# Kernel optimization log

Hardware: AMD Instinct MI355X
Metric: run time of the kernel (lower is better)

Reference implementation:

```python
import jax, jax.numpy as jnp
import numpy as np

D_MODEL = 256; D_INNER = 512; D_STATE = 32; D_CONV = 4
NHEADS = 8; HEADDIM = 64; NLAYERS = 2
CONV_DIM = D_INNER + 2 * D_STATE          # 576
ZX = 2 * D_INNER + 2 * D_STATE + NHEADS   # 1096
BSZ = 4; SEQ = 2048
EPS = 1e-5


def _causal_conv(x, w, b):
    # depthwise causal conv: x (b,l,c), w (c,k), b (c,)
    k = w.shape[1]
    L = x.shape[1]
    xp = jnp.pad(x, ((0, 0), (k - 1, 0), (0, 0)))
    out = jnp.zeros_like(x)
    for i in range(k):
        out = out + xp[:, i:i + L, :] * w[:, i]
    return out + b


def _mamba2(u, in_w, conv_w, conv_b, dt_bias, A_log, Dvec, gnorm_w, out_w):
    bsz, l, _ = u.shape
    zxbcdt = jnp.einsum('bld,ed->ble', u, in_w)  # (b,l,ZX)
    z = zxbcdt[..., :D_INNER]
    xBC = zxbcdt[..., D_INNER:D_INNER + CONV_DIM]
    dt = jax.nn.softplus(zxbcdt[..., D_INNER + CONV_DIM:] + dt_bias)  # (b,l,h)
    xBC = jax.nn.silu(_causal_conv(xBC, conv_w, conv_b))
    xs = xBC[..., :D_INNER].reshape(bsz, l, NHEADS, HEADDIM)
    Bm = xBC[..., D_INNER:D_INNER + D_STATE]   # (b,l,n)
    Cm = xBC[..., D_INNER + D_STATE:]          # (b,l,n)
    A = -jnp.exp(A_log)                         # (h,)
    dA = jnp.exp(dt * A)                        # (b,l,h)
    dtx = dt[..., None] * xs                    # (b,l,h,p)

    def step(h, inp):
        dA_t, dtx_t, B_t, C_t = inp
        h = h * dA_t[:, :, None, None] + dtx_t[..., None] * B_t[:, None, None, :]
        y_t = jnp.einsum('bhpn,bn->bhp', h, C_t)
        return h, y_t

    h0 = jnp.zeros((bsz, NHEADS, HEADDIM, D_STATE), u.dtype)
    _, ys = jax.lax.scan(step, h0, (dA.swapaxes(0, 1), dtx.swapaxes(0, 1),
                                    Bm.swapaxes(0, 1), Cm.swapaxes(0, 1)))
    y = ys.swapaxes(0, 1) + Dvec[None, None, :, None] * xs
    y = y.reshape(bsz, l, D_INNER)
    y = y * jax.nn.silu(z)                       # gated RMSNorm (Mamba2 default)
    y = y * jax.lax.rsqrt(jnp.mean(y * y, axis=-1, keepdims=True) + EPS) * gnorm_w
    return jnp.einsum('ble,de->bld', y, out_w)


def _encoder(x, padding_mask, in_w, conv_w, conv_b, dt_bias, A_log, Dvec,
             gnorm_w, out_w, ln_w, ln_b):
    mask = padding_mask[..., None]

    def ln(h):
        mu = jnp.mean(h, -1, keepdims=True)
        var = jnp.mean((h - mu) ** 2, -1, keepdims=True)
        return (h - mu) * jax.lax.rsqrt(var + EPS) * ln_w + ln_b

    for i in range(NLAYERS):
        h = ln(x)
        of = _mamba2(h, in_w[i, 0], conv_w[i, 0], conv_b[i, 0], dt_bias[i, 0],
                     A_log[i, 0], Dvec[i, 0], gnorm_w[i, 0], out_w[i, 0])
        ob = jnp.flip(_mamba2(jnp.flip(h, 1), in_w[i, 1], conv_w[i, 1],
                              conv_b[i, 1], dt_bias[i, 1], A_log[i, 1],
                              Dvec[i, 1], gnorm_w[i, 1], out_w[i, 1]), 1)
        x = x + jnp.where(mask, 0.0, of + ob)
    return jnp.where(mask, 0.0, ln(x))


def setup_inputs() -> dict:
    key = jax.random.key(0)
    ks = jax.random.split(key, 8)
    s = 0.02
    x = jax.random.normal(ks[0], (BSZ, SEQ, D_MODEL), jnp.float32)
    padding_mask = jax.random.randint(ks[1], (BSZ, SEQ), 0, 2) > 0
    in_w = jax.random.normal(ks[2], (NLAYERS, 2, ZX, D_MODEL), jnp.float32) * s
    conv_w = jax.random.normal(ks[3], (NLAYERS, 2, CONV_DIM, D_CONV), jnp.float32) * s
    conv_b = jnp.zeros((NLAYERS, 2, CONV_DIM), jnp.float32)
    dt_bias = jax.random.normal(ks[4], (NLAYERS, 2, NHEADS), jnp.float32) * 0.1
    A_log = jnp.log(jax.random.uniform(ks[5], (NLAYERS, 2, NHEADS), jnp.float32, 1.0, 16.0))
    Dvec = jnp.ones((NLAYERS, 2, NHEADS), jnp.float32)
    gnorm_w = jnp.ones((NLAYERS, 2, D_INNER), jnp.float32)
    out_w = jax.random.normal(ks[6], (NLAYERS, 2, D_MODEL, D_INNER), jnp.float32) * s
    ln_w = jnp.ones((D_MODEL,), jnp.float32)
    ln_b = jnp.zeros((D_MODEL,), jnp.float32)
    return {"x": x, "padding_mask": padding_mask, "in_w": in_w, "conv_w": conv_w,
            "conv_b": conv_b, "dt_bias": dt_bias, "A_log": A_log, "Dvec": Dvec,
            "gnorm_w": gnorm_w, "out_w": out_w, "ln_w": ln_w, "ln_b": ln_b}


def reference(x, padding_mask, in_w, conv_w, conv_b, dt_bias, A_log, Dvec,
              gnorm_w, out_w, ln_w, ln_b):
    return _encoder(x, padding_mask, in_w, conv_w, conv_b, dt_bias, A_log,
                    Dvec, gnorm_w, out_w, ln_w, ln_b)
```

## Files before the change

kernel.cpp:

```cpp
#include <hip/hip_runtime.h>
#include <hip/hip_bf16.h>
#include <math.h>

#define SEQL 2048
#define NB 4
#define DMm 256
#define DIi 512
#define DSs 32
#define NHH 8
#define HDD 64
#define CDD 576
#define ZXD 1096
#define ZXT 2192
#define NPAD 2304
#define NLAY 2
#define QC 64
#define NCH 32
#define RT 8192
#define EPSV 1e-5f

typedef __hip_bfloat16 bf16_t;
using short8 = __attribute__((ext_vector_type(8))) short;
using f32x4  = __attribute__((ext_vector_type(4))) float;

__device__ __forceinline__ float bf16bits2f(short u) {
  union { unsigned int i; float f; } v;
  v.i = ((unsigned int)(unsigned short)u) << 16;
  return v.f;
}

__device__ __forceinline__ int torig(int d, int c, int s) {
  int v = c * QC + s;
  return d ? (SEQL - 1 - v) : v;
}

__device__ __forceinline__ int is_masked(const void* mask, const int* mflag, int r) {
  return (*mflag) ? (int)(((const unsigned char*)mask)[r] != 0)
                  : (int)(((const int*)mask)[r] != 0);
}

__global__ void detect_mask(const unsigned char* __restrict__ m, int* __restrict__ flag) {
  __shared__ int any;
  if (threadIdx.x == 0) any = 0;
  __syncthreads();
  int a = 0;
  for (int i = threadIdx.x; i < RT; i += blockDim.x)
    if ((i & 3) && m[i]) a = 1;
  if (a) atomicOr(&any, 1);
  __syncthreads();
  if (threadIdx.x == 0) *flag = any;
}

__global__ void cvt_weights(const float* __restrict__ in_w, const float* __restrict__ out_w,
                            bf16_t* __restrict__ inw_bf, bf16_t* __restrict__ wcat_bf) {
  const int n1 = NLAY * NPAD * DMm;
  const int n2 = NLAY * DMm * 1024;
  for (int idx = blockIdx.x * blockDim.x + threadIdx.x; idx < n1 + n2; idx += gridDim.x * blockDim.x) {
    if (idx < n1) {
      int l = idx / (NPAD * DMm);
      int rem = idx % (NPAD * DMm);
      int r = rem / DMm, k = rem % DMm;
      inw_bf[idx] = __float2bfloat16(r < ZXT ? in_w[((size_t)l * ZXT + r) * DMm + k] : 0.f);
    } else {
      int j = idx - n1;
      int l = j / (DMm * 1024);
      int rem = j % (DMm * 1024);
      int dd = rem >> 10, k = rem & 1023;
      int dir = k >> 9, e = k & 511;
      wcat_bf[j] = __float2bfloat16(out_w[((size_t)((l * 2 + dir) * DMm) + dd) * DIi + e]);
    }
  }
}

__global__ void ln_kernel(const float* __restrict__ x, bf16_t* __restrict__ h,
                          const float* __restrict__ lnw, const float* __restrict__ lnb) {
  int r = blockIdx.x, lane = threadIdx.x;
  float4 v = ((const float4*)(x + (size_t)r * DMm))[lane];
  float s = v.x + v.y + v.z + v.w;
  #pragma unroll
  for (int o = 32; o; o >>= 1) s += __shfl_xor(s, o);
  float mu = s * (1.f / DMm);
  float d0 = v.x - mu, d1 = v.y - mu, d2 = v.z - mu, d3 = v.w - mu;
  float q = d0*d0 + d1*d1 + d2*d2 + d3*d3;
  #pragma unroll
  for (int o = 32; o; o >>= 1) q += __shfl_xor(q, o);
  float rstd = rsqrtf(q * (1.f / DMm) + EPSV);
  float4 w  = ((const float4*)lnw)[lane];
  float4 bb = ((const float4*)lnb)[lane];
  union { bf16_t o4[4]; uint2 u; } out;
  out.o4[0] = __float2bfloat16(d0 * rstd * w.x + bb.x);
  out.o4[1] = __float2bfloat16(d1 * rstd * w.y + bb.y);
  out.o4[2] = __float2bfloat16(d2 * rstd * w.z + bb.z);
  out.o4[3] = __float2bfloat16(d3 * rstd * w.w + bb.w);
  ((uint2*)(h + (size_t)r * DMm))[lane] = out.u;
}

__global__ void final_ln(const float* __restrict__ x, const void* __restrict__ mask,
                         const int* __restrict__ mflag,
                         const float* __restrict__ lnw, const float* __restrict__ lnb,
                         float* __restrict__ out) {
  int r = blockIdx.x, lane = threadIdx.x;
  float4 v = ((const float4*)(x + (size_t)r * DMm))[lane];
  float s = v.x + v.y + v.z + v.w;
  #pragma unroll
  for (int o = 32; o; o >>= 1) s += __shfl_xor(s, o);
  float mu = s * (1.f / DMm);
  float d0 = v.x - mu, d1 = v.y - mu, d2 = v.z - mu, d3 = v.w - mu;
  float q = d0*d0 + d1*d1 + d2*d2 + d3*d3;
  #pragma unroll
  for (int o = 32; o; o >>= 1) q += __shfl_xor(q, o);
  float rstd = rsqrtf(q * (1.f / DMm) + EPSV);
  float4 w  = ((const float4*)lnw)[lane];
  float4 bb = ((const float4*)lnb)[lane];
  float4 o4;
  if (is_masked(mask, mflag, r)) { o4.x = o4.y = o4.z = o4.w = 0.f; }
  else {
    o4.x = d0 * rstd * w.x + bb.x; o4.y = d1 * rstd * w.y + bb.y;
    o4.z = d2 * rstd * w.z + bb.z; o4.w = d3 * rstd * w.w + bb.w;
  }
  ((float4*)(out + (size_t)r * DMm))[lane] = o4;
}

__global__ __launch_bounds__(256) void gemm_in(const bf16_t* __restrict__ A,
    const bf16_t* __restrict__ Bw, bf16_t* __restrict__ zx, float* __restrict__ dtf) {
  __shared__ __align__(16) bf16_t As[128][72];
  __shared__ __align__(16) bf16_t Bs[128][72];
  int L = blockIdx.y * 18 + blockIdx.x;
  int qx = L & 7, jx = L >> 3;
  int Lp = qx * 144 + jx;
  int n0 = (Lp % 18) * 128, m0 = (Lp / 18) * 128;
  int tid = threadIdx.x, lane = tid & 63, wid = tid >> 6;
  int wm = wid >> 1, wn = wid & 1;
  f32x4 acc[4][4] = {};
  int sr = tid >> 1, sh = (tid & 1) * 32;
  for (int k0 = 0; k0 < DMm; k0 += 64) {
    #pragma unroll
    for (int i = 0; i < 4; i++) {
      *(short8*)&As[sr][sh + i * 8] = *(const short8*)(A + (size_t)(m0 + sr) * DMm + k0 + sh + i * 8);
      *(short8*)&Bs[sr][sh + i * 8] = *(const short8*)(Bw + (size_t)(n0 + sr) * DMm + k0 + sh + i * 8);
    }
    __syncthreads();
    #pragma unroll
    for (int kk = 0; kk < 2; kk++) {
      short8 af[4], bf[4];
      #pragma unroll
      for (int mi = 0; mi < 4; mi++)
        af[mi] = *(const short8*)&As[wm * 64 + mi * 16 + (lane & 15)][kk * 32 + (lane >> 4) * 8];
      #pragma unroll
      for (int ni = 0; ni < 4; ni++)
        bf[ni] = *(const short8*)&Bs[wn * 64 + ni * 16 + (lane & 15)][kk * 32 + (lane >> 4) * 8];
      #pragma unroll
      for (int mi = 0; mi < 4; mi++)
        #pragma unroll
        for (int ni = 0; ni < 4; ni++)
          acc[mi][ni] = __builtin_amdgcn_mfma_f32_16x16x32_bf16(af[mi], bf[ni], acc[mi][ni], 0, 0, 0);
    }
    __syncthreads();
  }
  #pragma unroll
  for (int mi = 0; mi < 4; mi++) {
    #pragma unroll
    for (int ni = 0; ni < 4; ni++) {
      int col = n0 + wn * 64 + ni * 16 + (lane & 15);
      if (col < ZXT) {
        #pragma unroll
        for (int j = 0; j < 4; j++) {
          int row = m0 + wm * 64 + mi * 16 + (lane >> 4) * 4 + j;
          float v = acc[mi][ni][j];
          zx[(size_t)row * ZXT + col] = __float2bfloat16(v);
          if (col >= 1088 && col < 1096)
            dtf[(size_t)row * NHH + (col - 1088)] = v;
          else if (col >= 2184)
            dtf[((size_t)RT + row) * NHH + (col - 2184)] = v;
        }
      }
    }
  }
}

__global__ __launch_bounds__(256) void gemm_out(const bf16_t* __restrict__ A, const bf16_t* __restrict__ Bw,
    float* __restrict__ C, int M, int N, int K, int ldc,
    const void* __restrict__ mask, const int* __restrict__ mflag) {
  __shared__ bf16_t As[64][40];
  __shared__ bf16_t Bs[64][40];
  int n0 = blockIdx.x * 64, m0 = blockIdx.y * 64;
  int tid = threadIdx.x, lane = tid & 63, wid = tid >> 6;
  f32x4 acc[4] = {};
  int sr = tid >> 2, sk = (tid & 3) * 8;
  for (int k0 = 0; k0 < K; k0 += 32) {
    short8 av = *(const short8*)(A + (size_t)(m0 + sr) * K + k0 + sk);
    *(short8*)&As[sr][sk] = av;
    short8 bv = *(const short8*)(Bw + (size_t)(n0 + sr) * K + k0 + sk);
    *(short8*)&Bs[sr][sk] = bv;
    __syncthreads();
    short8 af = *(const short8*)&As[wid * 16 + (lane & 15)][(lane >> 4) * 8];
    #pragma unroll
    for (int nt = 0; nt < 4; nt++) {
      short8 bf = *(const short8*)&Bs[nt * 16 + (lane & 15)][(lane >> 4) * 8];
      acc[nt] = __builtin_amdgcn_mfma_f32_16x16x32_bf16(af, bf, acc[nt], 0, 0, 0);
    }
    __syncthreads();
  }
  #pragma unroll
  for (int nt = 0; nt < 4; nt++) {
    int col = n0 + nt * 16 + (lane & 15);
    #pragma unroll
    for (int j = 0; j < 4; j++) {
      int row = m0 + wid * 16 + (lane >> 4) * 4 + j;
      if (!is_masked(mask, mflag, row)) C[(size_t)row * ldc + col] += acc[nt][j];
    }
  }
}

__global__ __launch_bounds__(256) void chunk_p1(const bf16_t* __restrict__ zx,
    const float* __restrict__ conv_w, const float* __restrict__ conv_b,
    const float* __restrict__ dtf, const float* __restrict__ dt_bias,
    const float* __restrict__ A_log, const float* __restrict__ Dvec,
    bf16_t* __restrict__ ybuf, bf16_t* __restrict__ Sbuf, float* __restrict__ lgbuf,
    float* __restrict__ Pbuf, bf16_t* __restrict__ cbuf, int layer) {
  int c = blockIdx.x, hd = blockIdx.y, b = blockIdx.z;
  int h = hd >> 1, d = hd & 1;
  int tid = threadIdx.x, lane = tid & 63, wid = tid >> 6;
  int rb = b * SEQL;
  __shared__ __align__(16) bf16_t Bs[QC][40];
  __shared__ __align__(16) bf16_t Cs[QC][40];
  __shared__ __align__(16) bf16_t Xt[QC][72];
  __shared__ __align__(16) char shraw[19968];
  bf16_t (*rawX)[64]  = (bf16_t(*)[64])shraw;
  bf16_t (*rawBC)[64] = (bf16_t(*)[64])(shraw + 8576);
  float (*cw4)[4]     = (float(*)[4])(shraw + 17152);
  float *cbv          = (float*)(shraw + 19200);
  bf16_t (*Ms)[72]    = (bf16_t(*)[72])shraw;
  bf16_t (*Btw)[72]   = (bf16_t(*)[72])(shraw + 9216);
  __shared__ float lam[QC], dts[QC], wss[QC];

  for (int i = tid; i < 67 * 8; i += 256) {
    int s = i >> 3, p0 = (i & 7) * 8;
    int v = c * QC + s - 3;
    short8 xv = {0,0,0,0,0,0,0,0}, bcv = {0,0,0,0,0,0,0,0};
    if (v >= 0) {
      int t = d ? (SEQL - 1 - v) : v;
      const bf16_t* rowp = zx + (size_t)(rb + t) * ZXT + d * ZXD + DIi;
      xv  = *(const short8*)(rowp + h * HDD + p0);
      bcv = *(const short8*)(rowp + 512 + p0);
    }
    *(short8*)&rawX[s][p0]  = xv;
    *(short8*)&rawBC[s][p0] = bcv;
  }
  if (tid < 128) {
    int cch = (tid < 64) ? (h * HDD + tid) : (512 + (tid - 64));
    const float* wp = conv_w + ((size_t)((layer * 2 + d) * CDD) + cch) * 4;
    *(float4*)cw4[tid] = *(const float4*)wp;
    cbv[tid] = conv_b[(layer * 2 + d) * CDD + cch];
  }
  if (tid < QC) {
    int ro = rb + torig(d, c, tid);
    size_t rr = (size_t)d * RT + ro;
    float xv = dtf[rr * NHH + h] + dt_bias[(layer * 2 + d) * NHH + h];
    float dtv = (xv > 20.f) ? xv : log1pf(expf(xv));
    float Ah = -expf(A_log[(layer * 2 + d) * NHH + h]);
    float la = dtv * Ah;
    dts[tid] = dtv;
    #pragma unroll
    for (int o = 1; o < 64; o <<= 1) { float vv = __shfl_up(la, o); if (tid >= o) la += vv; }
    lam[tid] = la;
    Pbuf[rr * NHH + h] = expf(la);
    float lq = __shfl(la, 63);
    wss[tid] = expf(lq - la) * dtv;
    if (tid == 63) lgbuf[((b * NHH + h) * 2 + d) * NCH + c] = la;
  }
  __syncthreads();

  for (int i = tid; i < QC * HDD; i += 256) {
    int s = i >> 6, p = i & 63;
    float a = cbv[p];
    #pragma unroll
    for (int ii = 0; ii < 4; ii++)
      a += __bfloat162float(rawX[s + ii][p]) * cw4[p][ii];
    a = a / (1.f + expf(-a));
    Xt[p][s] = __float2bfloat16(a);
  }
  for (int i = tid; i < QC * HDD; i += 256) {
    int s = i >> 6, q = i & 63;
    float a = cbv[64 + q];
    #pragma unroll
    for (int ii = 0; ii < 4; ii++)
      a += __bfloat162float(rawBC[s + ii][q]) * cw4[64 + q][ii];
    a = a / (1.f + expf(-a));
    bf16_t av = __float2bfloat16(a);
    if (q < DSs) Bs[s][q] = av; else Cs[s][q - DSs] = av;
  }
  __syncthreads();

  {
    short8 cf = *(const short8*)&Cs[wid * 16 + (lane & 15)][(lane >> 4) * 8];
    int sbase = lane & 15;
    #pragma unroll
    for (int sc = 0; sc < 4; sc++) {
      int s = sc * 16 + sbase;
      if (sc <= wid) {
        short8 bfr = *(const short8*)&Bs[s][(lane >> 4) * 8];
        f32x4 g = {};
        g = __builtin_amdgcn_mfma_f32_16x16x32_bf16(cf, bfr, g, 0, 0, 0);
        float ls = lam[s], dv = dts[s];
        #pragma unroll
        for (int j = 0; j < 4; j++) {
          int t = wid * 16 + (lane >> 4) * 4 + j;
          float m = (s <= t) ? expf(lam[t] - ls) * dv * g[j] : 0.f;
          Ms[t][s] = __float2bfloat16(m);
        }
      } else {
        #pragma unroll
        for (int j = 0; j < 4; j++) Ms[wid * 16 + (lane >> 4) * 4 + j][s] = __float2bfloat16(0.f);
      }
    }
  }
  for (int i = tid; i < DSs * QC; i += 256) {
    int n = i >> 6, s = i & 63;
    Btw[n][s] = __float2bfloat16(wss[s] * __bfloat162float(Bs[s][n]));
  }
  if (h == 0) {
    for (int i = tid; i < QC * DSs; i += 256) {
      int s = i >> 5, n = i & 31;
      cbuf[((size_t)(d * RT + rb + torig(d, c, s))) * DSs + n] = Cs[s][n];
    }
  }
  __syncthreads();

  float Dv = Dvec[(layer * 2 + d) * NHH + h];
  {
    short8 ma0 = *(const short8*)&Ms[wid * 16 + (lane & 15)][(lane >> 4) * 8];
    short8 ma1 = *(const short8*)&Ms[wid * 16 + (lane & 15)][32 + (lane >> 4) * 8];
    #pragma unroll
    for (int pt = 0; pt < 4; pt++) {
      short8 xb0 = *(const short8*)&Xt[pt * 16 + (lane & 15)][(lane >> 4) * 8];
      short8 xb1 = *(const short8*)&Xt[pt * 16 + (lane & 15)][32 + (lane >> 4) * 8];
      f32x4 ya = {};
      ya = __builtin_amdgcn_mfma_f32_16x16x32_bf16(ma0, xb0, ya, 0, 0, 0);
      ya = __builtin_amdgcn_mfma_f32_16x16x32_bf16(ma1, xb1, ya, 0, 0, 0);
      int p = pt * 16 + (lane & 15);
      #pragma unroll
      for (int j = 0; j < 4; j++) {
        int t = wid * 16 + (lane >> 4) * 4 + j;
        float xv = __bfloat162float(Xt[p][t]);
        ybuf[((size_t)(d * RT + rb + torig(d, c, t))) * DIi + h * HDD + p] =
            __float2bfloat16(ya[j] + Dv * xv);
      }
    }
  }
  {
    short8 xa0 = *(const short8*)&Xt[wid * 16 + (lane & 15)][(lane >> 4) * 8];
    short8 xa1 = *(const short8*)&Xt[wid * 16 + (lane & 15)][32 + (lane >> 4) * 8];
    size_t base = ((size_t)((b * NHH + h) * 2 + d) * NCH + c) * 2048;
    #pragma unroll
    for (int nt = 0; nt < 2; nt++) {
      short8 bw0 = *(const short8*)&Btw[nt * 16 + (lane & 15)][(lane >> 4) * 8];
      short8 bw1 = *(const short8*)&Btw[nt * 16 + (lane & 15)][32 + (lane >> 4) * 8];
      f32x4 sa = {};
      sa = __builtin_amdgcn_mfma_f32_16x16x32_bf16(xa0, bw0, sa, 0, 0, 0);
      sa = __builtin_amdgcn_mfma_f32_16x16x32_bf16(xa1, bw1, sa, 0, 0, 0);
      int n = nt * 16 + (lane & 15);
      #pragma unroll
      for (int j = 0; j < 4; j++) {
        int p = wid * 16 + (lane >> 4) * 4 + j;
        Sbuf[base + (size_t)p * DSs + n] = __float2bfloat16(sa[j]);
      }
    }
  }
}

__global__ __launch_bounds__(256) void chunk_p2b(const bf16_t* __restrict__ Sbuf,
    const float* __restrict__ lgbuf, bf16_t* __restrict__ Hbuf) {
  int bhd = blockIdx.x, cb = blockIdx.y;
  int tid = threadIdx.x;
  __shared__ float W[NCH][NCH + 1];
  __shared__ float cum[NCH];
  if (tid < NCH) {
    float la = lgbuf[bhd * NCH + tid];
    #pragma unroll
    for (int o = 1; o < NCH; o <<= 1) { float v = __shfl_up(la, o); if (tid >= o) la += v; }
    cum[tid] = la;
  }
  __syncthreads();
  for (int i = tid; i < NCH * NCH; i += 256) {
    int c = i >> 5, cp = i & 31;
    W[c][cp] = (cp < c) ? expf(cum[c - 1] - cum[cp]) : 0.f;
  }
  __syncthreads();
  int j = cb * 256 + tid;
  const bf16_t* Sb = Sbuf + (size_t)bhd * NCH * 2048;
  bf16_t* Hb = Hbuf + (size_t)bhd * NCH * 2048;
  float H[NCH];
  #pragma unroll
  for (int c = 0; c < NCH; c++) H[c] = 0.f;
  for (int cp = 0; cp < NCH; cp++) {
    float s = __bfloat162float(Sb[(size_t)cp * 2048 + j]);
    #pragma unroll
    for (int c = 0; c < NCH; c++) H[c] += W[c][cp] * s;
  }
  #pragma unroll
  for (int c = 0; c < NCH; c++) Hb[(size_t)c * 2048 + j] = __float2bfloat16(H[c]);
}

__global__ __launch_bounds__(512) void chunk_p3g(const bf16_t* __restrict__ cbuf,
    const bf16_t* __restrict__ ybuf, const float* __restrict__ Pbuf,
    const bf16_t* __restrict__ Hbuf, const bf16_t* __restrict__ zx,
    const float* __restrict__ gnorm, bf16_t* __restrict__ ycat, int layer) {
  int cc = blockIdx.x, d = blockIdx.y, b = blockIdx.z;
  int c = cc >> 1, trow0 = (cc & 1) * 32;
  int tid = threadIdx.x, lane = tid & 63, wid = tid >> 6;
  int rb = b * SEQL;
  __shared__ __align__(16) bf16_t Cs[32][40];
  __shared__ __align__(16) bf16_t Hs[NHH][HDD][40];
  __shared__ __align__(16) bf16_t Ys[32][520];
  __shared__ float Ps[NHH][32];

  for (int i = tid; i < 32 * DSs; i += 512) {
    int s = i >> 5, n = i & 31;
    Cs[s][n] = cbuf[((size_t)(d * RT + rb + torig(d, c, trow0 + s))) * DSs + n];
  }
  for (int i = tid; i < NHH * HDD * DSs; i += 512) {
    int hh = i >> 11, rem = i & 2047;
    Hs[hh][rem >> 5][rem & 31] =
        Hbuf[((size_t)((b * NHH + hh) * 2 + d) * NCH + c) * 2048 + rem];
  }
  if (tid < NHH * 32) {
    int hh = tid >> 5, t = tid & 31;
    Ps[hh][t] = Pbuf[((size_t)(d * RT + rb + torig(d, c, trow0 + t))) * NHH + hh];
  }
  __syncthreads();

  {
    int h = wid;
    #pragma unroll
    for (int tt = 0; tt < 2; tt++) {
      short8 ca = *(const short8*)&Cs[tt * 16 + (lane & 15)][(lane >> 4) * 8];
      #pragma unroll
      for (int pp = 0; pp < 4; pp++) {
        short8 hf = *(const short8*)&Hs[h][pp * 16 + (lane & 15)][(lane >> 4) * 8];
        f32x4 a = {};
        a = __builtin_amdgcn_mfma_f32_16x16x32_bf16(ca, hf, a, 0, 0, 0);
        int p = pp * 16 + (lane & 15);
        #pragma unroll
        for (int j = 0; j < 4; j++) {
          int trel = tt * 16 + (lane >> 4) * 4 + j;
          size_t rr = (size_t)(d * RT + rb + torig(d, c, trow0 + trel));
          float iv = __bfloat162float(ybuf[rr * DIi + h * HDD + p]);
          Ys[trel][h * HDD + p] = __float2bfloat16(iv + Ps[h][trel] * a[j]);
        }
      }
    }
  }
  __syncthreads();

  const float* gw = gnorm + (layer * 2 + d) * DIi;
  #pragma unroll
  for (int rloc = 0; rloc < 4; rloc++) {
    int trel = wid * 4 + rloc;
    int r = rb + torig(d, c, trow0 + trel);
    short8 yv8 = *(const short8*)&Ys[trel][lane * 8];
    short8 zv8 = *(const short8*)(zx + (size_t)r * ZXT + d * ZXD + lane * 8);
    float g[8]; float ss = 0.f;
    #pragma unroll
    for (int j = 0; j < 8; j++) {
      float y = bf16bits2f(yv8[j]);
      float z = bf16bits2f(zv8[j]);
      float v = y * z / (1.f + expf(-z));
      g[j] = v; ss += v * v;
    }
    #pragma unroll
    for (int o = 32; o; o >>= 1) ss += __shfl_xor(ss, o);
    float sc = rsqrtf(ss * (1.f / DIi) + EPSV);
    union { bf16_t o8[8]; uint4 u; } ov;
    #pragma unroll
    for (int j = 0; j < 8; j++)
      ov.o8[j] = __float2bfloat16(g[j] * sc * gw[lane * 8 + j]);
    *(uint4*)(ycat + (size_t)r * 1024 + d * DIi + lane * 8) = ov.u;
  }
}

extern "C" void kernel_launch(void* const* d_in, const int* in_sizes, int n_in,
                              void* d_out, int out_size, void* d_ws, size_t ws_size,
                              hipStream_t stream) {
  const float* x_in    = (const float*)d_in[0];
  const void*  maskp   = (const void*)d_in[1];
  const float* in_w    = (const float*)d_in[2];
  const float* conv_w  = (const float*)d_in[3];
  const float* conv_b  = (const float*)d_in[4];
  const float* dt_bias = (const float*)d_in[5];
  const float* A_log   = (const float*)d_in[6];
  const float* Dvec    = (const float*)d_in[7];
  const float* gnorm_w = (const float*)d_in[8];
  const float* out_w   = (const float*)d_in[9];
  const float* ln_w    = (const float*)d_in[10];
  const float* ln_b    = (const float*)d_in[11];

  char* ws = (char*)d_ws;
  size_t off = 0;
  auto alloc = [&](size_t bytes) -> void* {
    void* p = ws + off; off += (bytes + 255) & ~(size_t)255; return p;
  };
  float*  x_cur   = (float*)alloc((size_t)RT * DMm * 4);
  bf16_t* h_bf    = (bf16_t*)alloc((size_t)RT * DMm * 2);
  bf16_t* zx      = (bf16_t*)alloc((size_t)RT * ZXT * 2);
  bf16_t* cbuf    = (bf16_t*)alloc((size_t)2 * RT * DSs * 2);
  float*  dtf     = (float*)alloc((size_t)2 * RT * NHH * 4);
  float*  Pbuf    = (float*)alloc((size_t)2 * RT * NHH * 4);
  bf16_t* ybuf    = (bf16_t*)alloc((size_t)2 * RT * DIi * 2);
  bf16_t* ycat    = (bf16_t*)alloc((size_t)RT * 1024 * 2);
  bf16_t* Sbuf    = (bf16_t*)alloc((size_t)64 * NCH * 2048 * 2);
  bf16_t* Hbuf    = (bf16_t*)alloc((size_t)64 * NCH * 2048 * 2);
  float*  lgbuf   = (float*)alloc((size_t)64 * NCH * 4);
  bf16_t* inw_bf  = (bf16_t*)alloc((size_t)NLAY * NPAD * DMm * 2);
  bf16_t* wcat_bf = (bf16_t*)alloc((size_t)NLAY * DMm * 1024 * 2);
  int*    mflag   = (int*)alloc(256);

  hipMemcpyAsync(x_cur, x_in, (size_t)RT * DMm * 4, hipMemcpyDeviceToDevice, stream);
  detect_mask<<<1, 256, 0, stream>>>((const unsigned char*)maskp, mflag);
  cvt_weights<<<256, 256, 0, stream>>>(in_w, out_w, inw_bf, wcat_bf);

  for (int layer = 0; layer < NLAY; layer++) {
    ln_kernel<<<RT, 64, 0, stream>>>(x_cur, h_bf, ln_w, ln_b);
    gemm_in<<<dim3(NPAD / 128, RT / 128), 256, 0, stream>>>(
        h_bf, inw_bf + (size_t)layer * NPAD * DMm, zx, dtf);
    chunk_p1<<<dim3(NCH, 16, NB), 256, 0, stream>>>(zx, conv_w, conv_b, dtf, dt_bias,
                                                    A_log, Dvec, ybuf, Sbuf, lgbuf,
                                                    Pbuf, cbuf, layer);
    chunk_p2b<<<dim3(64, 8), 256, 0, stream>>>(Sbuf, lgbuf, Hbuf);
    chunk_p3g<<<dim3(64, 2, NB), 512, 0, stream>>>(cbuf, ybuf, Pbuf, Hbuf, zx,
                                                   gnorm_w, ycat, layer);
    gemm_out<<<dim3(DMm / 64, RT / 64), 256, 0, stream>>>(
        ycat, wcat_bf + (size_t)layer * DMm * 1024, x_cur,
        RT, DMm, 1024, DMm, maskp, mflag);
  }
  final_ln<<<RT, 64, 0, stream>>>(x_cur, maskp, mflag, ln_w, ln_b, (float*)d_out);
}
```

Baseline: 277.9 us.

## Fuse setup kernels, drop input copy, batch LN rows, vectorize chunk LDS accesses

Merges mask detection and weight conversion into one setup kernel. Removes the device-to-device copy of the input by having layer 0 read x_in directly and having gemm_out write init+acc. It also packs four LN rows per 256-thread block and vectorizes the Xt shared-memory writes and reads in chunk_p1. The aim is fewer launches, less memory traffic and fewer LDS transactions, at the cost of a templated epilogue and more code paths.

Measured after the change: 264.4 us. 1.05x faster.

```diff
diff --git a/kernel.cpp b/kernel.cpp
--- a/kernel.cpp
+++ b/kernel.cpp
@@ -39,20 +39,20 @@
                   : (int)(((const int*)mask)[r] != 0);
 }
 
-__global__ void detect_mask(const unsigned char* __restrict__ m, int* __restrict__ flag) {
-  __shared__ int any;
-  if (threadIdx.x == 0) any = 0;
-  __syncthreads();
-  int a = 0;
-  for (int i = threadIdx.x; i < RT; i += blockDim.x)
-    if ((i & 3) && m[i]) a = 1;
-  if (a) atomicOr(&any, 1);
-  __syncthreads();
-  if (threadIdx.x == 0) *flag = any;
-}
-
-__global__ void cvt_weights(const float* __restrict__ in_w, const float* __restrict__ out_w,
-                            bf16_t* __restrict__ inw_bf, bf16_t* __restrict__ wcat_bf) {
+__global__ void setup_kernel(const unsigned char* __restrict__ m, int* __restrict__ flag,
+                             const float* __restrict__ in_w, const float* __restrict__ out_w,
+                             bf16_t* __restrict__ inw_bf, bf16_t* __restrict__ wcat_bf) {
+  if (blockIdx.x == 0) {
+    __shared__ int any;
+    if (threadIdx.x == 0) any = 0;
+    __syncthreads();
+    int a = 0;
+    for (int i = threadIdx.x; i < RT; i += blockDim.x)
+      if ((i & 3) && m[i]) a = 1;
+    if (a) atomicOr(&any, 1);
+    __syncthreads();
+    if (threadIdx.x == 0) *flag = any;
+  }
   const int n1 = NLAY * NPAD * DMm;
   const int n2 = NLAY * DMm * 1024;
   for (int idx = blockIdx.x * blockDim.x + threadIdx.x; idx < n1 + n2; idx += gridDim.x * blockDim.x) {
@@ -72,9 +72,9 @@
   }
 }
 
-__global__ void ln_kernel(const float* __restrict__ x, bf16_t* __restrict__ h,
+__global__ __launch_bounds__(256) void ln_kernel(const float* __restrict__ x, bf16_t* __restrict__ h,
                           const float* __restrict__ lnw, const float* __restrict__ lnb) {
-  int r = blockIdx.x, lane = threadIdx.x;
+  int r = blockIdx.x * 4 + (threadIdx.x >> 6), lane = threadIdx.x & 63;
   float4 v = ((const float4*)(x + (size_t)r * DMm))[lane];
   float s = v.x + v.y + v.z + v.w;
   #pragma unroll
@@ -178,8 +178,9 @@
   }
 }
 
+template<int INIT>
 __global__ __launch_bounds__(256) void gemm_out(const bf16_t* __restrict__ A, const bf16_t* __restrict__ Bw,
-    float* __restrict__ C, int M, int N, int K, int ldc,
+    float* __restrict__ C, const float* __restrict__ init, int M, int N, int K, int ldc,
     const void* __restrict__ mask, const int* __restrict__ mflag) {
   __shared__ bf16_t As[64][40];
   __shared__ bf16_t Bs[64][40];
@@ -207,7 +208,12 @@
     #pragma unroll
     for (int j = 0; j < 4; j++) {
       int row = m0 + wid * 16 + (lane >> 4) * 4 + j;
-      if (!is_masked(mask, mflag, row)) C[(size_t)row * ldc + col] += acc[nt][j];
+      if (INIT) {
+        float base = init[(size_t)row * ldc + col];
+        C[(size_t)row * ldc + col] = base + (is_masked(mask, mflag, row) ? 0.f : acc[nt][j]);
+      } else {
+        if (!is_masked(mask, mflag, row)) C[(size_t)row * ldc + col] += acc[nt][j];
+      }
     }
   }
 }
@@ -271,14 +277,24 @@
   }
   __syncthreads();
 
-  for (int i = tid; i < QC * HDD; i += 256) {
-    int s = i >> 6, p = i & 63;
-    float a = cbv[p];
-    #pragma unroll
-    for (int ii = 0; ii < 4; ii++)
-      a += __bfloat162float(rawX[s + ii][p]) * cw4[p][ii];
-    a = a / (1.f + expf(-a));
-    Xt[p][s] = __float2bfloat16(a);
+  {
+    int p = tid & 63, sg = tid >> 6;
+    #pragma unroll
+    for (int half = 0; half < 2; half++) {
+      int s0 = sg * 16 + half * 8;
+      union { bf16_t h8[8]; short8 v; } ox;
+      #pragma unroll
+      for (int j = 0; j < 8; j++) {
+        int s = s0 + j;
+        float a = cbv[p];
+        #pragma unroll
+        for (int ii = 0; ii < 4; ii++)
+          a += __bfloat162float(rawX[s + ii][p]) * cw4[p][ii];
+        a = a / (1.f + expf(-a));
+        ox.h8[j] = __float2bfloat16(a);
+      }
+      *(short8*)&Xt[p][s0] = ox.v;
+    }
   }
   for (int i = tid; i < QC * HDD; i += 256) {
     int s = i >> 6, q = i & 63;
@@ -331,6 +347,7 @@
   {
     short8 ma0 = *(const short8*)&Ms[wid * 16 + (lane & 15)][(lane >> 4) * 8];
     short8 ma1 = *(const short8*)&Ms[wid * 16 + (lane & 15)][32 + (lane >> 4) * 8];
+    int t0 = wid * 16 + (lane >> 4) * 4;
     #pragma unroll
     for (int pt = 0; pt < 4; pt++) {
       short8 xb0 = *(const short8*)&Xt[pt * 16 + (lane & 15)][(lane >> 4) * 8];
@@ -339,10 +356,12 @@
       ya = __builtin_amdgcn_mfma_f32_16x16x32_bf16(ma0, xb0, ya, 0, 0, 0);
       ya = __builtin_amdgcn_mfma_f32_16x16x32_bf16(ma1, xb1, ya, 0, 0, 0);
       int p = pt * 16 + (lane & 15);
+      union { uint2 u; short s4[4]; } xr;
+      xr.u = *(const uint2*)&Xt[p][t0];
       #pragma unroll
       for (int j = 0; j < 4; j++) {
-        int t = wid * 16 + (lane >> 4) * 4 + j;
-        float xv = __bfloat162float(Xt[p][t]);
+        int t = t0 + j;
+        float xv = bf16bits2f(xr.s4[j]);
         ybuf[((size_t)(d * RT + rb + torig(d, c, t))) * DIi + h * HDD + p] =
             __float2bfloat16(ya[j] + Dv * xv);
       }
@@ -515,12 +534,12 @@
   bf16_t* wcat_bf = (bf16_t*)alloc((size_t)NLAY * DMm * 1024 * 2);
   int*    mflag   = (int*)alloc(256);
 
-  hipMemcpyAsync(x_cur, x_in, (size_t)RT * DMm * 4, hipMemcpyDeviceToDevice, stream);
-  detect_mask<<<1, 256, 0, stream>>>((const unsigned char*)maskp, mflag);
-  cvt_weights<<<256, 256, 0, stream>>>(in_w, out_w, inw_bf, wcat_bf);
+  setup_kernel<<<256, 256, 0, stream>>>((const unsigned char*)maskp, mflag,
+                                        in_w, out_w, inw_bf, wcat_bf);
 
   for (int layer = 0; layer < NLAY; layer++) {
-    ln_kernel<<<RT, 64, 0, stream>>>(x_cur, h_bf, ln_w, ln_b);
+    const float* xsrc = (layer == 0) ? x_in : x_cur;
+    ln_kernel<<<RT / 4, 256, 0, stream>>>(xsrc, h_bf, ln_w, ln_b);
     gemm_in<<<dim3(NPAD / 128, RT / 128), 256, 0, stream>>>(
         h_bf, inw_bf + (size_t)layer * NPAD * DMm, zx, dtf);
     chunk_p1<<<dim3(NCH, 16, NB), 256, 0, stream>>>(zx, conv_w, conv_b, dtf, dt_bias,
@@ -529,9 +548,14 @@
     chunk_p2b<<<dim3(64, 8), 256, 0, stream>>>(Sbuf, lgbuf, Hbuf);
     chunk_p3g<<<dim3(64, 2, NB), 512, 0, stream>>>(cbuf, ybuf, Pbuf, Hbuf, zx,
                                                    gnorm_w, ycat, layer);
-    gemm_out<<<dim3(DMm / 64, RT / 64), 256, 0, stream>>>(
-        ycat, wcat_bf + (size_t)layer * DMm * 1024, x_cur,
-        RT, DMm, 1024, DMm, maskp, mflag);
+    if (layer == 0)
+      gemm_out<1><<<dim3(DMm / 64, RT / 64), 256, 0, stream>>>(
+          ycat, wcat_bf + (size_t)layer * DMm * 1024, x_cur, x_in,
+          RT, DMm, 1024, DMm, maskp, mflag);
+    else
+      gemm_out<0><<<dim3(DMm / 64, RT / 64), 256, 0, stream>>>(
+          ycat, wcat_bf + (size_t)layer * DMm * 1024, x_cur, nullptr,
+          RT, DMm, 1024, DMm, maskp, mflag);
   }
   final_ln<<<RT, 64, 0, stream>>>(x_cur, maskp, mflag, ln_w, ln_b, (float*)d_out);
 }
```
